# Kernel optimization log

Hardware: AMD Instinct MI355X
Metric: run time of the kernel (lower is better)

## Reference

```python
import jax, jax.numpy as jnp
import numpy as np

H, NH, KVH = 2048, 16, 4
HD = H // NH            # 128
GROUPS = NH // KVH      # 4
E, TOPK = 8, 2
I_MOE, I_SH = 1408, 5632
THETA = 1000000.0
EPS = 1e-6
B, S = 1, 1024


def rms_norm(x, w):
    var = jnp.mean(jnp.square(x), axis=-1, keepdims=True)
    return x * jax.lax.rsqrt(var + EPS) * w


def rotate_half(x):
    x1, x2 = jnp.split(x, 2, axis=-1)
    return jnp.concatenate([-x2, x1], axis=-1)


def apply_rope(q, k, position_ids):
    # q: [B,S,NH,HD], k: [B,S,KVH,HD]
    inv_freq = 1.0 / (THETA ** (jnp.arange(0, HD, 2, dtype=jnp.float32) / HD))
    ang = position_ids.astype(jnp.float32)[..., None] * inv_freq  # [B,S,HD/2]
    emb = jnp.concatenate([ang, ang], axis=-1)                    # [B,S,HD]
    cos = jnp.cos(emb)[:, :, None, :]
    sin = jnp.sin(emb)[:, :, None, :]
    q = q * cos + rotate_half(q) * sin
    k = k * cos + rotate_half(k) * sin
    return q, k


def setup_inputs() -> dict:
    key = jax.random.key(0)
    ks = jax.random.split(key, 24)
    sd = 0.02
    inp = {
        "hidden_states": jax.random.normal(ks[0], (B, S, H), jnp.float32),
        "position_ids": jnp.arange(S, dtype=jnp.int32)[None, :].repeat(B, 0),
        "ln1_w": jnp.ones((H,), jnp.float32),
        "ln2_w": jnp.ones((H,), jnp.float32),
        "q_w": jax.random.normal(ks[1], (H, NH * HD), jnp.float32) * sd,
        "q_b": jnp.zeros((NH * HD,), jnp.float32),
        "k_w": jax.random.normal(ks[2], (H, KVH * HD), jnp.float32) * sd,
        "k_b": jnp.zeros((KVH * HD,), jnp.float32),
        "v_w": jax.random.normal(ks[3], (H, KVH * HD), jnp.float32) * sd,
        "v_b": jnp.zeros((KVH * HD,), jnp.float32),
        "o_w": jax.random.normal(ks[4], (NH * HD, H), jnp.float32) * sd,
        "router_w": jax.random.normal(ks[5], (H, E), jnp.float32) * sd,
        "e_gate": jax.random.normal(ks[6], (E, H, I_MOE), jnp.float32) * sd,
        "e_up": jax.random.normal(ks[7], (E, H, I_MOE), jnp.float32) * sd,
        "e_down": jax.random.normal(ks[8], (E, I_MOE, H), jnp.float32) * sd,
        "s_gate": jax.random.normal(ks[9], (H, I_SH), jnp.float32) * sd,
        "s_up": jax.random.normal(ks[10], (H, I_SH), jnp.float32) * sd,
        "s_down": jax.random.normal(ks[11], (I_SH, H), jnp.float32) * sd,
        "sg_w": jax.random.normal(ks[12], (H, 1), jnp.float32) * sd,
    }
    return inp


def attention(x, position_ids, q_w, q_b, k_w, k_b, v_w, v_b, o_w):
    b, s, _ = x.shape
    q = (x @ q_w + q_b).reshape(b, s, NH, HD)
    k = (x @ k_w + k_b).reshape(b, s, KVH, HD)
    v = (x @ v_w + v_b).reshape(b, s, KVH, HD)
    q, k = apply_rope(q, k, position_ids)
    # GQA: repeat kv heads
    k = jnp.repeat(k, GROUPS, axis=2)  # [b,s,NH,HD]
    v = jnp.repeat(v, GROUPS, axis=2)
    scale = HD ** -0.5
    scores = jnp.einsum("bqhd,bkhd->bhqk", q, k) * scale
    causal = jnp.tril(jnp.ones((s, s), bool))
    scores = jnp.where(causal[None, None], scores, jnp.finfo(scores.dtype).min)
    probs = jax.nn.softmax(scores, axis=-1)
    out = jnp.einsum("bhqk,bkhd->bqhd", probs, v).reshape(b, s, NH * HD)
    return out @ o_w


def sparse_moe(x, router_w, e_gate, e_up, e_down, s_gate, s_up, s_down, sg_w):
    b, s, h = x.shape
    xf = x.reshape(b * s, h)  # [T,H]
    T = b * s
    probs = jax.nn.softmax(xf @ router_w, axis=-1)        # [T,E]
    top_w, top_i = jax.lax.top_k(probs, TOPK)             # norm_topk_prob=False
    weights = jnp.zeros((T, E), xf.dtype).at[jnp.arange(T)[:, None], top_i].set(top_w)
    g = jax.nn.silu(jnp.einsum("th,ehi->eti", xf, e_gate))
    u = jnp.einsum("th,ehi->eti", xf, e_up)
    d = jnp.einsum("eti,eih->eth", g * u, e_down)         # [E,T,H]
    moe_out = jnp.einsum("eth,te->th", d, weights)
    shared = (jax.nn.silu(xf @ s_gate) * (xf @ s_up)) @ s_down
    shared = shared * jax.nn.sigmoid(xf @ sg_w)
    return (moe_out + shared).reshape(b, s, h)


def reference(hidden_states, position_ids, ln1_w, ln2_w, q_w, q_b, k_w, k_b,
              v_w, v_b, o_w, router_w, e_gate, e_up, e_down,
              s_gate, s_up, s_down, sg_w):
    h = hidden_states
    attn = attention(rms_norm(h, ln1_w), position_ids,
                     q_w, q_b, k_w, k_b, v_w, v_b, o_w)
    h = h + attn
    moe = sparse_moe(rms_norm(h, ln2_w), router_w, e_gate, e_up, e_down,
                     s_gate, s_up, s_down, sg_w)
    return h + moe
```

## Files before the change

### kernel.cpp

```cpp
#include <hip/hip_runtime.h>
#include <hip/hip_bf16.h>

#define S_ 1024
#define H_ 2048
#define NH_ 16
#define KVH_ 4
#define HD_ 128
#define IM_ 1408
#define ISH_ 5632
#define E_ 8

typedef __bf16 bf16x8 __attribute__((ext_vector_type(8)));
typedef float f32x4 __attribute__((ext_vector_type(4)));

typedef unsigned int __attribute__((address_space(1))) as1_u32;
typedef unsigned int __attribute__((address_space(3))) as3_u32;

__device__ __forceinline__ void gload16(const void* g, void* l) {
  __builtin_amdgcn_global_load_lds((const as1_u32*)g, (as3_u32*)l, 16, 0, 0);
}

__device__ __forceinline__ short f2bf(float f) {
  unsigned u = __float_as_uint(f);
  u = u + 0x7FFFu + ((u >> 16) & 1u);
  return (short)(u >> 16);
}

__device__ __forceinline__ f32x4 mfma16(bf16x8 a, bf16x8 b, f32x4 c) {
  return __builtin_amdgcn_mfma_f32_16x16x32_bf16(a, b, c, 0, 0, 0);
}

template<bool MAXOP>
__device__ __forceinline__ float block_reduce(float v, float* sbuf) {
  #pragma unroll
  for (int o = 32; o >= 1; o >>= 1) {
    float t = __shfl_down(v, o);
    v = MAXOP ? fmaxf(v, t) : (v + t);
  }
  int lane = threadIdx.x & 63, w = threadIdx.x >> 6;
  if (lane == 0) sbuf[w] = v;
  __syncthreads();
  float r = sbuf[0];
  #pragma unroll
  for (int i = 1; i < 4; i++) r = MAXOP ? fmaxf(r, sbuf[i]) : (r + sbuf[i]);
  __syncthreads();
  return r;
}

struct TransDesc {
  const float* src; short* dst;
  int R, C, tx, perz, base;
  long long srcZ, dstZ;
};
struct TransAll { TransDesc d[10]; };

#define TGRP 1096

__global__ __launch_bounds__(256) void mega_k(TransAll ta, int transBlocks,
                                              const int* pos_ids, float* ct, float* st,
                                              const float* qb, const float* kb, const float* vb,
                                              float* qkv, float* attn_f, int* counts,
                                              const float* hidden, const float* ln1_w,
                                              short* x1, float* h2) {
  __shared__ float tile[4 * TGRP];
  __shared__ float sbuf[4];
  const int bid = blockIdx.x;
  const int t = threadIdx.x;
  if (bid < transBlocks) {
    int w = 0;
    #pragma unroll
    for (int i = 1; i < 10; i++) if (bid >= ta.d[i].base) w = i;
    const TransDesc& D = ta.d[w];
    int local = bid - D.base;
    int z = local / D.perz, rem = local - z * D.perz;
    int by = rem / D.tx, bx = rem - by * D.tx;
    const float* src = D.src + (long long)z * D.srcZ;
    short* dst = D.dst + (long long)z * D.dstZ;
    const int r0 = by * 64, c0 = bx * 64;
    const int C = D.C, R = D.R;
    #pragma unroll
    for (int i = 0; i < 4; i++) {
      int idx = t + i * 256;
      int row = idx >> 4, c4 = (idx & 15) * 4;
      f32x4 v = __builtin_nontemporal_load(
          (const f32x4*)&src[(size_t)(r0 + row) * C + c0 + c4]);
      *(f32x4*)&tile[(row >> 4) * TGRP + (row & 15) * 68 + c4] = v;
    }
    __syncthreads();
    const int col = t >> 2, seg = t & 3;
    const float* tp = &tile[seg * TGRP + col];
    short outv[16];
    #pragma unroll
    for (int j = 0; j < 16; j++)
      outv[j] = f2bf(tp[j * 68]);
    short* dp = &dst[(size_t)(c0 + col) * R + r0 + seg * 16];
    *(int4*)dp = *(const int4*)&outv[0];
    *(int4*)(dp + 8) = *(const int4*)&outv[8];
  } else if (bid < transBlocks + 5376) {
    int pb = bid - transBlocks;
    if (pb == 0 && t < 16) counts[t] = 0;
    if (pb < 256) {
      int i = pb * 256 + t;
      int p = i >> 6, f = i & 63;
      float pos = (float)pos_ids[p];
      float inv = powf(1.0e6f, -(float)f * (1.f / 64.f));
      float a = pos * inv;
      ct[i] = cosf(a); st[i] = sinf(a);
    } else if (pb < 3328) {
      int idx = (pb - 256) * 256 + t;
      int j = (idx * 4) % 3072;
      float4 v;
      const float* b = (j < 2048) ? qb + j : ((j < 2560) ? kb + (j - 2048) : vb + (j - 2560));
      v.x = b[0]; v.y = b[1]; v.z = b[2]; v.w = b[3];
      ((float4*)qkv)[idx] = v;
    } else {
      int idx = (pb - 3328) * 256 + t;
      ((float4*)attn_f)[idx] = (float4){0.f, 0.f, 0.f, 0.f};
    }
  } else {
    int tr = bid - transBlocks - 5376;
    const float* xr = hidden + (long long)tr * H_;
    float ss = 0.f;
    for (int i = t; i < H_ / 4; i += 256) {
      float4 v = ((const float4*)xr)[i];
      ss += v.x * v.x + v.y * v.y + v.z * v.z + v.w * v.w;
    }
    ss = block_reduce<false>(ss, sbuf);
    float rs = rsqrtf(ss * (1.f / (float)H_) + 1e-6f);
    for (int i = t; i < H_; i += 256) {
      float xv = xr[i];
      x1[(long long)tr * H_ + i] = f2bf(xv * rs * ln1_w[i]);
      h2[(long long)tr * H_ + i] = xv;
    }
  }
}

struct GemmP {
  const short* A; long long strideA; int adiv; int lda;
  const short* B; long long strideB; int bdiv; int ldb;
  void* C; long long strideC; int cdiv; int ldc;
  const int* e_off; const int* e_cnt;
  const int* list; const float* scale;
  float alpha;
  int M, N, K;
  int cskip, ckb;
  int ksplit, kchunk;
  int upoff;
};

template<int EPI>
__device__ __forceinline__ void gemm_body(const GemmP& p, int bx, int by, int bz,
                                          short* As, short* Bs) {
  constexpr bool FUSED = (EPI == 6 || EPI == 7);
  constexpr bool GATH  = (EPI == 7);
  constexpr int BM = 128, BN = 128, BK = 32;
  const int zo = bz / p.ksplit;
  const int kc = bz - zo * p.ksplit;
  const int m0 = by * BM;
  const int n0 = bx * (FUSED ? 64 : BN);
  if (FUSED && n0 >= p.N) return;

  int off = 0, cnt = p.M;
  if constexpr (EPI == 4 || GATH) {
    off = p.e_off[zo]; cnt = p.e_cnt[zo];
    if (m0 >= cnt) return;
  }
  if (p.cskip && n0 >= m0 + BM) return;
  int kend = p.ckb ? min(m0 + BM, p.K) : p.K;
  const int kbeg = kc * p.kchunk;
  kend = min(kend, kbeg + p.kchunk);
  if (kbeg >= kend) return;

  const short* Ab = p.A + (long long)(zo / p.adiv) * p.strideA;
  const short* Bb = p.B + (long long)(zo / p.bdiv) * p.strideB;

  const int tid = threadIdx.x;
  const int lane = tid & 63, wid = tid >> 6;
  const int wr = wid >> 1, wc = wid & 1;
  const int kg = lane >> 4, li = lane & 15;

  const int srow = tid >> 2;
  const int scol = (((tid & 3) ^ ((tid >> 3) & 3))) * 8;
  const short* aSrc[2];
  const short* bSrc[2];
  #pragma unroll
  for (int c = 0; c < 2; c++) {
    int ra = srow + c * 64;
    int gr;
    if constexpr (GATH)          { int rr = m0 + ra; if (rr >= cnt) rr = cnt - 1; gr = p.list[off + rr]; }
    else if constexpr (EPI == 4) { int rr = m0 + ra; if (rr >= cnt) rr = cnt - 1; gr = off + rr; }
    else                         gr = m0 + ra;
    aSrc[c] = Ab + (long long)gr * p.lda + scol;
    int br = FUSED ? (n0 + srow + (c ? p.upoff : 0)) : (n0 + srow + c * 64);
    bSrc[c] = Bb + (long long)br * p.ldb + scol;
  }

  f32x4 acc[4][4];
  #pragma unroll
  for (int i = 0; i < 4; i++)
    #pragma unroll
    for (int j = 0; j < 4; j++) acc[i][j] = (f32x4){0.f, 0.f, 0.f, 0.f};

  #pragma unroll
  for (int c = 0; c < 2; c++) {
    gload16(aSrc[c] + kbeg, &As[tid * 8 + c * 2048]);
    gload16(bSrc[c] + kbeg, &Bs[tid * 8 + c * 2048]);
  }
  __syncthreads();

  const int kgx = kg ^ ((li >> 1) & 3);
  int brow[4];
  #pragma unroll
  for (int nj = 0; nj < 4; nj++)
    brow[nj] = FUSED ? (((nj & 2) ? 64 : 0) + wc * 32 + (nj & 1) * 16 + li)
                     : (wc * 64 + nj * 16 + li);

  int cur = 0;
  for (int k0 = kbeg; k0 < kend; k0 += BK) {
    const int nk = k0 + BK;
    if (nk < kend) {
      #pragma unroll
      for (int c = 0; c < 2; c++) {
        gload16(aSrc[c] + nk, &As[(cur ^ 1) * 4096 + tid * 8 + c * 2048]);
        gload16(bSrc[c] + nk, &Bs[(cur ^ 1) * 4096 + tid * 8 + c * 2048]);
      }
    }
    bf16x8 av[4], bv[4];
    #pragma unroll
    for (int mi = 0; mi < 4; mi++)
      av[mi] = *(const bf16x8*)&As[cur * 4096 + (wr * 64 + mi * 16 + li) * BK + kgx * 8];
    #pragma unroll
    for (int nj = 0; nj < 4; nj++)
      bv[nj] = *(const bf16x8*)&Bs[cur * 4096 + brow[nj] * BK + kgx * 8];
    #pragma unroll
    for (int mi = 0; mi < 4; mi++)
      #pragma unroll
      for (int nj = 0; nj < 4; nj++)
        acc[mi][nj] = mfma16(av[mi], bv[nj], acc[mi][nj]);
    __syncthreads();
    cur ^= 1;
  }

  const long long zc = (long long)(zo / p.cdiv) * p.strideC;
  if constexpr (FUSED) {
    short* C = (short*)p.C;
    #pragma unroll
    for (int mi = 0; mi < 4; mi++) {
      #pragma unroll
      for (int nj = 0; nj < 2; nj++) {
        #pragma unroll
        for (int r = 0; r < 4; r++) {
          int ml = wr * 64 + mi * 16 + kg * 4 + r;
          int mg = m0 + ml;
          int ng = n0 + wc * 32 + nj * 16 + li;
          float g = acc[mi][nj][r], u = acc[mi][nj + 2][r];
          float gu = g * (1.f / (1.f + __expf(-g))) * u;
          if constexpr (GATH) {
            if (mg < cnt) C[(long long)(off + mg) * p.ldc + ng] = f2bf(gu);
          } else {
            C[(long long)mg * p.ldc + ng] = f2bf(gu);
          }
        }
      }
    }
  } else {
    #pragma unroll
    for (int mi = 0; mi < 4; mi++) {
      #pragma unroll
      for (int nj = 0; nj < 4; nj++) {
        #pragma unroll
        for (int r = 0; r < 4; r++) {
          int ml = wr * 64 + mi * 16 + kg * 4 + r;
          int nl2 = wc * 64 + nj * 16 + li;
          int mg = m0 + ml, ng = n0 + nl2;
          float v = acc[mi][nj][r] * p.alpha;
          if constexpr (EPI == 0) {
            float* C = (float*)p.C + zc;
            __builtin_nontemporal_store(v, &C[(long long)mg * p.ldc + ng]);
          } else if constexpr (EPI == 1) {
            float* C = (float*)p.C + zc;
            atomicAdd(&C[(long long)mg * p.ldc + ng], v);
          } else if constexpr (EPI == 4) {
            if (mg < cnt) {
              float* C = (float*)p.C;
              int tok = p.list[off + mg];
              atomicAdd(&C[(long long)tok * p.ldc + ng], p.scale[off + mg] * v);
            }
          } else if constexpr (EPI == 5) {
            float* C = (float*)p.C;
            atomicAdd(&C[(long long)mg * p.ldc + ng], p.scale[mg] * v);
          }
        }
      }
    }
  }
}

template<int EPI>
__global__ __launch_bounds__(256) void gemm_bt(GemmP p) {
  __shared__ __align__(16) short As[2 * 128 * 32];
  __shared__ __align__(16) short Bs[2 * 128 * 32];
  gemm_body<EPI>(p, blockIdx.x, blockIdx.y, blockIdx.z, As, Bs);
}

__global__ __launch_bounds__(256) void gemm_gu_dual(GemmP pe, GemmP ps) {
  __shared__ __align__(16) short As[2 * 128 * 32];
  __shared__ __align__(16) short Bs[2 * 128 * 32];
  int z = blockIdx.z;
  if (z < E_) gemm_body<7>(pe, blockIdx.x, blockIdx.y, z, As, Bs);
  else        gemm_body<6>(ps, (z - E_) * 22 + blockIdx.x, blockIdx.y, 0, As, Bs);
}

template<int EPI1, int EPI2>
__global__ __launch_bounds__(256) void gemm_dual(GemmP p1, GemmP p2, int z1) {
  __shared__ __align__(16) short As[2 * 128 * 32];
  __shared__ __align__(16) short Bs[2 * 128 * 32];
  int z = blockIdx.z;
  if (z < z1) gemm_body<EPI1>(p1, blockIdx.x, blockIdx.y, z, As, Bs);
  else        gemm_body<EPI2>(p2, blockIdx.x, blockIdx.y, z - z1, As, Bs);
}

__global__ __launch_bounds__(256) void rmsnorm_k(const float* x, const float* w, short* o,
                                                 float* copy_out, float* rs_out) {
  __shared__ float sbuf[4];
  int t = blockIdx.x;
  const float* xr = x + (long long)t * H_;
  float ss = 0.f;
  for (int i = threadIdx.x; i < H_ / 4; i += 256) {
    float4 v = ((const float4*)xr)[i];
    ss += v.x * v.x + v.y * v.y + v.z * v.z + v.w * v.w;
  }
  ss = block_reduce<false>(ss, sbuf);
  float rs = rsqrtf(ss * (1.f / (float)H_) + 1e-6f);
  for (int i = threadIdx.x; i < H_; i += 256) {
    float xv = xr[i];
    o[(long long)t * H_ + i] = f2bf(xv * rs * w[i]);
    if (copy_out) copy_out[(long long)t * H_ + i] = xv;
  }
  if (rs_out && threadIdx.x == 0) rs_out[t] = rs;
}

__global__ __launch_bounds__(256) void rope_fused_k(const float* qkv, short* qr, short* kr,
                                                    short* vt, const float* ct, const float* st) {
  int i = blockIdx.x * 256 + threadIdx.x;
  if (i < 2097152) {
    int t = i >> 11, j = i & 2047;
    int d = j & 127, f = d & 63;
    float c = ct[t * 64 + f], s = st[t * 64 + f];
    const float* row = qkv + (long long)t * 3072;
    float xv = row[j];
    float ov = (d < 64) ? -row[j + 64] : row[j - 64];
    qr[i] = f2bf(xv * c + ov * s);
  } else if (i < 2621440) {
    int j = i - 2097152;
    int t = j >> 9, jj = j & 511;
    int d = jj & 127, f = d & 63;
    float c = ct[t * 64 + f], s = st[t * 64 + f];
    const float* row = qkv + (long long)t * 3072 + 2048;
    float xv = row[jj];
    float ov = (d < 64) ? -row[jj + 64] : row[jj - 64];
    kr[j] = f2bf(xv * c + ov * s);
  } else {
    int j = i - 2621440;
    int kvh = j >> 17, rem = j & 131071;
    int d = rem >> 10, s_ = rem & 1023;
    vt[j] = f2bf(qkv[(long long)s_ * 3072 + 2560 + kvh * 128 + d]);
  }
}

__global__ __launch_bounds__(256) void cvt_bf16_k(const float* src, short* dst, int total) {
  int i = blockIdx.x * 256 + threadIdx.x;
  if (i < total) dst[i] = f2bf(src[i]);
}

__global__ __launch_bounds__(256) void softmax_k(const float* sc, short* P) {
  __shared__ float sbuf[4];
  long long row = blockIdx.x;
  int q = (int)(row & (S_ - 1));
  const float* sr = sc + row * S_;
  short* pr = P + row * S_;
  int L = q + 1;
  int Lcap = (q & ~127) + 128;
  float mx = -3.4e38f;
  for (int i = threadIdx.x; i < L; i += 256) mx = fmaxf(mx, sr[i]);
  mx = block_reduce<true>(mx, sbuf);
  float s = 0.f;
  for (int i = threadIdx.x; i < L; i += 256) s += __expf(sr[i] - mx);
  s = block_reduce<false>(s, sbuf);
  float inv = 1.f / s;
  for (int i = threadIdx.x; i < Lcap; i += 256) {
    float pv = (i < L) ? __expf(sr[i] - mx) * inv : 0.f;
    pr[i] = f2bf(pv);
  }
}

__global__ void router_k(const float* h2, const float* rs, const float* w2,
                         const float* rw, const float* sgw,
                         int* top_i, float* top_w, float* sg_sig, int* counts) {
  int t = blockIdx.x;
  int l = threadIdx.x;
  float le[8] = {0, 0, 0, 0, 0, 0, 0, 0};
  float ls = 0.f;
  float r = rs[t];
  for (int k = l; k < H_; k += 64) {
    float xv = h2[(long long)t * H_ + k] * r * w2[k];
    ls += xv * sgw[k];
    const float* rk = rw + k * E_;
    #pragma unroll
    for (int e = 0; e < E_; e++) le[e] += xv * rk[e];
  }
  #pragma unroll
  for (int o = 32; o >= 1; o >>= 1) {
    ls += __shfl_down(ls, o);
    #pragma unroll
    for (int e = 0; e < E_; e++) le[e] += __shfl_down(le[e], o);
  }
  if (l == 0) {
    float m = le[0];
    for (int e = 1; e < E_; e++) m = fmaxf(m, le[e]);
    float pe[8], s = 0.f;
    for (int e = 0; e < E_; e++) { pe[e] = __expf(le[e] - m); s += pe[e]; }
    float inv = 1.f / s;
    for (int e = 0; e < E_; e++) pe[e] *= inv;
    int i1 = 0;
    for (int e = 1; e < E_; e++) if (pe[e] > pe[i1]) i1 = e;
    int i2 = -1;
    for (int e = 0; e < E_; e++) if (e != i1 && (i2 < 0 || pe[e] > pe[i2])) i2 = e;
    top_i[2 * t] = i1; top_i[2 * t + 1] = i2;
    top_w[2 * t] = pe[i1]; top_w[2 * t + 1] = pe[i2];
    sg_sig[t] = 1.f / (1.f + __expf(-ls));
    atomicAdd(&counts[i1], 1); atomicAdd(&counts[i2], 1);
  }
}

__global__ void scan_k(const int* counts, int* offs) {
  if (threadIdx.x == 0 && blockIdx.x == 0) {
    int s = 0;
    for (int e = 0; e < E_; e++) { offs[e] = s; s += counts[e]; }
  }
}

__global__ __launch_bounds__(256) void fill_k(const int* top_i, const float* top_w, const int* offs,
                                              int* pos, int* list, float* pw) {
  int t = blockIdx.x * 256 + threadIdx.x;
  if (t >= S_) return;
  for (int j = 0; j < 2; j++) {
    int e = top_i[2 * t + j];
    int p_ = atomicAdd(&pos[e], 1);
    int slot = offs[e] + p_;
    list[slot] = t; pw[slot] = top_w[2 * t + j];
  }
}

static GemmP mkp() {
  GemmP p{};
  p.adiv = 1; p.bdiv = 1; p.cdiv = 1; p.alpha = 1.f;
  p.ksplit = 1; p.kchunk = 1 << 30;
  p.upoff = 0;
  return p;
}

extern "C" void kernel_launch(void* const* d_in, const int* in_sizes, int n_in,
                              void* d_out, int out_size, void* d_ws, size_t ws_size,
                              hipStream_t stream) {
  const float* hidden   = (const float*)d_in[0];
  const int*   pos_ids  = (const int*)d_in[1];
  const float* ln1_w    = (const float*)d_in[2];
  const float* ln2_w    = (const float*)d_in[3];
  const float* q_w      = (const float*)d_in[4];
  const float* q_b      = (const float*)d_in[5];
  const float* k_w      = (const float*)d_in[6];
  const float* k_b      = (const float*)d_in[7];
  const float* v_w      = (const float*)d_in[8];
  const float* v_b      = (const float*)d_in[9];
  const float* o_w      = (const float*)d_in[10];
  const float* router_w = (const float*)d_in[11];
  const float* e_gate   = (const float*)d_in[12];
  const float* e_up     = (const float*)d_in[13];
  const float* e_down   = (const float*)d_in[14];
  const float* s_gate   = (const float*)d_in[15];
  const float* s_up     = (const float*)d_in[16];
  const float* s_down   = (const float*)d_in[17];
  const float* sg_w     = (const float*)d_in[18];
  float* out = (float*)d_out;

  char* base = (char*)d_ws;
  size_t off_ = 0;
  auto alc = [&](size_t nbytes) -> char* {
    off_ = (off_ + 255) & ~(size_t)255;
    char* p = base + off_;
    off_ += nbytes;
    return p;
  };
  short* qkvT = (short*)alc((size_t)3072 * H_ * 2);
  short* oT   = (short*)alc((size_t)H_ * H_ * 2);
  short* eguT = (short*)alc((size_t)E_ * 2816 * H_ * 2);
  short* edT  = (short*)alc((size_t)E_ * H_ * IM_ * 2);
  short* sguT = (short*)alc((size_t)11264 * H_ * 2);
  short* sdT  = (short*)alc((size_t)H_ * ISH_ * 2);
  short* x1      = (short*)alc((size_t)S_ * H_ * 2);
  float* qkv_f   = (float*)alc((size_t)S_ * 3072 * 4);
  float* ct      = (float*)alc((size_t)S_ * 64 * 4);
  float* st      = (float*)alc((size_t)S_ * 64 * 4);
  short* qr      = (short*)alc((size_t)S_ * H_ * 2);
  short* kr      = (short*)alc((size_t)S_ * 512 * 2);
  short* vt      = (short*)alc((size_t)S_ * 512 * 2);
  float* attn_f  = (float*)alc((size_t)S_ * H_ * 4);
  short* attn    = (short*)alc((size_t)S_ * H_ * 2);
  float* h2      = (float*)alc((size_t)S_ * H_ * 4);
  short* x2      = (short*)alc((size_t)S_ * H_ * 2);
  float* rs2     = (float*)alc(S_ * 4);
  int*   top_i   = (int*)alc(2 * S_ * 4);
  float* top_w   = (float*)alc(2 * S_ * 4);
  float* sg_sig  = (float*)alc(S_ * 4);
  int*   counts  = (int*)alc(64);
  int*   pos     = counts + 8;
  int*   offs    = (int*)alc(32);
  int*   list    = (int*)alc(2 * S_ * 4);
  float* pw      = (float*)alc(2 * S_ * 4);
  char*  region  = alc(100663296);
  float* scores  = (float*)region;
  short* P       = (short*)(region + 67108864);
  short* gu_moeB = (short*)region;
  short* gushB   = (short*)(region + 16777216);

  {
    TransAll ta{};
    int b = 0;
    auto add = [&](int i, const float* s, short* d, int R, int C, int tz,
                   long long sZ, long long dZ) {
      int tx = C / 64, ty = R / 64;
      ta.d[i] = TransDesc{s, d, R, C, tx, tx * ty, b, sZ, dZ};
      b += tx * ty * tz;
    };
    add(0, q_w, qkvT, H_, H_, 1, 0, 0);
    add(1, k_w, qkvT + (size_t)2048 * H_, H_, 512, 1, 0, 0);
    add(2, v_w, qkvT + (size_t)2560 * H_, H_, 512, 1, 0, 0);
    add(3, o_w, oT, H_, H_, 1, 0, 0);
    add(4, e_gate, eguT, H_, IM_, E_, (long long)H_ * IM_, (long long)2816 * H_);
    add(5, e_up, eguT + (size_t)1408 * H_, H_, IM_, E_, (long long)H_ * IM_, (long long)2816 * H_);
    add(6, e_down, edT, IM_, H_, E_, (long long)IM_ * H_, (long long)IM_ * H_);
    add(7, s_gate, sguT, H_, ISH_, 1, 0, 0);
    add(8, s_up, sguT + (size_t)5632 * H_, H_, ISH_, 1, 0, 0);
    add(9, s_down, sdT, ISH_, H_, 1, 0, 0);
    mega_k<<<b + 5376 + 1024, 256, 0, stream>>>(ta, b, pos_ids, ct, st, q_b, k_b, v_b,
                                                qkv_f, attn_f, counts,
                                                hidden, ln1_w, x1, h2);
  }

  {
    GemmP p = mkp();
    p.A = x1; p.lda = H_;
    p.B = qkvT; p.ldb = H_;
    p.C = qkv_f; p.ldc = 3072;
    p.M = S_; p.N = 3072; p.K = H_;
    p.ksplit = 4; p.kchunk = 512;
    gemm_bt<1><<<dim3(24, 8, 4), 256, 0, stream>>>(p);
  }

  rope_fused_k<<<12288, 256, 0, stream>>>(qkv_f, qr, kr, vt, ct, st);

  {
    GemmP p = mkp();
    p.A = qr; p.strideA = HD_; p.lda = H_;
    p.B = kr; p.strideB = HD_; p.bdiv = 4; p.ldb = 512;
    p.C = scores; p.strideC = (long long)S_ * S_; p.ldc = S_;
    p.alpha = 0.08838834764831845f;
    p.M = S_; p.N = S_; p.K = HD_; p.cskip = 1;
    p.kchunk = HD_;
    gemm_bt<0><<<dim3(8, 8, NH_), 256, 0, stream>>>(p);
  }
  softmax_k<<<NH_ * S_, 256, 0, stream>>>(scores, P);
  {
    GemmP p = mkp();
    p.A = P; p.strideA = (long long)S_ * S_; p.lda = S_;
    p.B = vt; p.strideB = (long long)HD_ * S_; p.bdiv = 4; p.ldb = S_;
    p.C = attn_f; p.strideC = HD_; p.ldc = H_;
    p.M = S_; p.N = HD_; p.K = S_; p.ckb = 1;
    p.ksplit = 4; p.kchunk = 256;
    gemm_bt<1><<<dim3(1, 8, NH_ * 4), 256, 0, stream>>>(p);
  }
  cvt_bf16_k<<<8192, 256, 0, stream>>>(attn_f, attn, S_ * H_);
  {
    GemmP p = mkp();
    p.A = attn; p.lda = H_;
    p.B = oT; p.ldb = H_;
    p.C = h2; p.ldc = H_;
    p.M = S_; p.N = H_; p.K = H_;
    p.ksplit = 4; p.kchunk = 512;
    gemm_bt<1><<<dim3(16, 8, 4), 256, 0, stream>>>(p);
  }

  rmsnorm_k<<<S_, 256, 0, stream>>>(h2, ln2_w, x2, out, rs2);

  router_k<<<S_, 64, 0, stream>>>(h2, rs2, ln2_w, router_w, sg_w, top_i, top_w, sg_sig, counts);
  scan_k<<<1, 1, 0, stream>>>(counts, offs);
  fill_k<<<4, 256, 0, stream>>>(top_i, top_w, offs, pos, list, pw);

  {
    GemmP pe = mkp();
    pe.A = x2; pe.lda = H_;
    pe.B = eguT; pe.strideB = (long long)2816 * H_; pe.ldb = H_;
    pe.C = gu_moeB; pe.ldc = IM_;
    pe.e_off = offs; pe.e_cnt = counts; pe.list = list;
    pe.M = S_; pe.N = IM_; pe.K = H_;
    pe.upoff = IM_;
    GemmP ps = mkp();
    ps.A = x2; ps.lda = H_;
    ps.B = sguT; ps.ldb = H_;
    ps.C = gushB; ps.ldc = ISH_;
    ps.M = S_; ps.N = ISH_; ps.K = H_;
    ps.upoff = ISH_;
    gemm_gu_dual<<<dim3(22, 8, 12), 256, 0, stream>>>(pe, ps);
  }

  {
    GemmP pe = mkp();
    pe.A = gu_moeB; pe.lda = IM_;
    pe.B = edT; pe.strideB = (long long)H_ * IM_; pe.ldb = IM_;
    pe.C = out; pe.ldc = H_;
    pe.e_off = offs; pe.e_cnt = counts; pe.list = list; pe.scale = pw;
    pe.M = S_; pe.N = H_; pe.K = IM_;
    pe.ksplit = 2; pe.kchunk = 704;
    GemmP ps = mkp();
    ps.A = gushB; ps.lda = ISH_;
    ps.B = sdT; ps.ldb = ISH_;
    ps.C = out; ps.ldc = H_; ps.scale = sg_sig;
    ps.M = S_; ps.N = H_; ps.K = ISH_;
    ps.ksplit = 4; ps.kchunk = 1408;
    gemm_dual<4, 5><<<dim3(16, 8, E_ * 2 + 4), 256, 0, stream>>>(pe, ps, E_ * 2);
  }
}
```

Before: 615.6 us.

## Replace atomic split-K with partial buffers reduced in consumer kernels

The QKV and output-projection GEMMs now use split-K of 2 and write plain stores into two partial buffers instead of atomically accumulating into pre-initialised outputs. The bias add and residual add move into the RoPE and a new fused RMSNorm kernel, which sum the partials. The PV GEMM drops split-K and writes bf16 directly, which removes the attn_f zeroing and the separate conversion kernel. This cuts atomics, memset-style initialisation and one kernel launch, at the cost of fewer blocks per GEMM and extra partial-buffer reads.

```diff
diff --git a/kernel.cpp b/kernel.cpp
--- a/kernel.cpp
+++ b/kernel.cpp
@@ -59,9 +59,9 @@
 __global__ __launch_bounds__(256) void mega_k(TransAll ta, int transBlocks,
                                               const int* pos_ids, float* ct, float* st,
                                               const float* qb, const float* kb, const float* vb,
-                                              float* qkv, float* attn_f, int* counts,
+                                              float* biasCat, int* counts,
                                               const float* hidden, const float* ln1_w,
-                                              short* x1, float* h2) {
+                                              short* x1) {
   __shared__ float tile[4 * TGRP];
   __shared__ float sbuf[4];
   const int bid = blockIdx.x;
@@ -96,29 +96,21 @@
     short* dp = &dst[(size_t)(c0 + col) * R + r0 + seg * 16];
     *(int4*)dp = *(const int4*)&outv[0];
     *(int4*)(dp + 8) = *(const int4*)&outv[8];
-  } else if (bid < transBlocks + 5376) {
+  } else if (bid < transBlocks + 256) {
     int pb = bid - transBlocks;
-    if (pb == 0 && t < 16) counts[t] = 0;
-    if (pb < 256) {
-      int i = pb * 256 + t;
-      int p = i >> 6, f = i & 63;
-      float pos = (float)pos_ids[p];
-      float inv = powf(1.0e6f, -(float)f * (1.f / 64.f));
-      float a = pos * inv;
-      ct[i] = cosf(a); st[i] = sinf(a);
-    } else if (pb < 3328) {
-      int idx = (pb - 256) * 256 + t;
-      int j = (idx * 4) % 3072;
-      float4 v;
-      const float* b = (j < 2048) ? qb + j : ((j < 2560) ? kb + (j - 2048) : vb + (j - 2560));
-      v.x = b[0]; v.y = b[1]; v.z = b[2]; v.w = b[3];
-      ((float4*)qkv)[idx] = v;
-    } else {
-      int idx = (pb - 3328) * 256 + t;
-      ((float4*)attn_f)[idx] = (float4){0.f, 0.f, 0.f, 0.f};
+    if (pb == 0) {
+      if (t < 16) counts[t] = 0;
+      for (int j = t; j < 3072; j += 256)
+        biasCat[j] = (j < 2048) ? qb[j] : ((j < 2560) ? kb[j - 2048] : vb[j - 2560]);
     }
+    int i = pb * 256 + t;
+    int p = i >> 6, f = i & 63;
+    float pos = (float)pos_ids[p];
+    float inv = powf(1.0e6f, -(float)f * (1.f / 64.f));
+    float a = pos * inv;
+    ct[i] = cosf(a); st[i] = sinf(a);
   } else {
-    int tr = bid - transBlocks - 5376;
+    int tr = bid - transBlocks - 256;
     const float* xr = hidden + (long long)tr * H_;
     float ss = 0.f;
     for (int i = t; i < H_ / 4; i += 256) {
@@ -130,7 +122,6 @@
     for (int i = t; i < H_; i += 256) {
       float xv = xr[i];
       x1[(long long)tr * H_ + i] = f2bf(xv * rs * ln1_w[i]);
-      h2[(long long)tr * H_ + i] = xv;
     }
   }
 }
@@ -275,11 +266,11 @@
           int mg = m0 + ml, ng = n0 + nl2;
           float v = acc[mi][nj][r] * p.alpha;
           if constexpr (EPI == 0) {
-            float* C = (float*)p.C + zc;
-            __builtin_nontemporal_store(v, &C[(long long)mg * p.ldc + ng]);
-          } else if constexpr (EPI == 1) {
-            float* C = (float*)p.C + zc;
-            atomicAdd(&C[(long long)mg * p.ldc + ng], v);
+            float* C = (float*)p.C + zc + (long long)kc * p.strideC;
+            C[(long long)mg * p.ldc + ng] = v;
+          } else if constexpr (EPI == 2) {
+            short* C = (short*)p.C + zc;
+            C[(long long)mg * p.ldc + ng] = f2bf(v);
           } else if constexpr (EPI == 4) {
             if (mg < cnt) {
               float* C = (float*)p.C;
@@ -320,57 +311,61 @@
   else        gemm_body<EPI2>(p2, blockIdx.x, blockIdx.y, z - z1, As, Bs);
 }
 
-__global__ __launch_bounds__(256) void rmsnorm_k(const float* x, const float* w, short* o,
-                                                 float* copy_out, float* rs_out) {
-  __shared__ float sbuf[4];
-  int t = blockIdx.x;
-  const float* xr = x + (long long)t * H_;
-  float ss = 0.f;
-  for (int i = threadIdx.x; i < H_ / 4; i += 256) {
-    float4 v = ((const float4*)xr)[i];
-    ss += v.x * v.x + v.y * v.y + v.z * v.z + v.w * v.w;
-  }
-  ss = block_reduce<false>(ss, sbuf);
-  float rs = rsqrtf(ss * (1.f / (float)H_) + 1e-6f);
-  for (int i = threadIdx.x; i < H_; i += 256) {
-    float xv = xr[i];
-    o[(long long)t * H_ + i] = f2bf(xv * rs * w[i]);
-    if (copy_out) copy_out[(long long)t * H_ + i] = xv;
-  }
-  if (rs_out && threadIdx.x == 0) rs_out[t] = rs;
-}
-
-__global__ __launch_bounds__(256) void rope_fused_k(const float* qkv, short* qr, short* kr,
+__global__ __launch_bounds__(256) void rope_fused_k(const float* p0, const float* p1,
+                                                    const float* bias, short* qr, short* kr,
                                                     short* vt, const float* ct, const float* st) {
   int i = blockIdx.x * 256 + threadIdx.x;
   if (i < 2097152) {
     int t = i >> 11, j = i & 2047;
     int d = j & 127, f = d & 63;
     float c = ct[t * 64 + f], s = st[t * 64 + f];
-    const float* row = qkv + (long long)t * 3072;
-    float xv = row[j];
-    float ov = (d < 64) ? -row[j + 64] : row[j - 64];
+    long long base = (long long)t * 3072;
+    float xv = p0[base + j] + p1[base + j] + bias[j];
+    int jo = (d < 64) ? j + 64 : j - 64;
+    float ov = p0[base + jo] + p1[base + jo] + bias[jo];
+    if (d < 64) ov = -ov;
     qr[i] = f2bf(xv * c + ov * s);
   } else if (i < 2621440) {
     int j = i - 2097152;
     int t = j >> 9, jj = j & 511;
     int d = jj & 127, f = d & 63;
     float c = ct[t * 64 + f], s = st[t * 64 + f];
-    const float* row = qkv + (long long)t * 3072 + 2048;
-    float xv = row[jj];
-    float ov = (d < 64) ? -row[jj + 64] : row[jj - 64];
+    long long base = (long long)t * 3072 + 2048;
+    float xv = p0[base + jj] + p1[base + jj] + bias[2048 + jj];
+    int jo = (d < 64) ? jj + 64 : jj - 64;
+    float ov = p0[base + jo] + p1[base + jo] + bias[2048 + jo];
+    if (d < 64) ov = -ov;
     kr[j] = f2bf(xv * c + ov * s);
   } else {
     int j = i - 2621440;
     int kvh = j >> 17, rem = j & 131071;
     int d = rem >> 10, s_ = rem & 1023;
-    vt[j] = f2bf(qkv[(long long)s_ * 3072 + 2560 + kvh * 128 + d]);
-  }
-}
-
-__global__ __launch_bounds__(256) void cvt_bf16_k(const float* src, short* dst, int total) {
-  int i = blockIdx.x * 256 + threadIdx.x;
-  if (i < total) dst[i] = f2bf(src[i]);
+    long long idx = (long long)s_ * 3072 + 2560 + kvh * 128 + d;
+    vt[j] = f2bf(p0[idx] + p1[idx] + bias[2560 + kvh * 128 + d]);
+  }
+}
+
+__global__ __launch_bounds__(256) void rmsnorm2f_k(const float* p0, const float* p1,
+                                                   const float* hid, const float* w,
+                                                   short* x2, float* outp, float* rs_out) {
+  __shared__ float rowbuf[H_];
+  __shared__ float sbuf[4];
+  int tr = blockIdx.x;
+  long long base = (long long)tr * H_;
+  float ss = 0.f;
+  for (int i = threadIdx.x; i < H_; i += 256) {
+    float hv = p0[base + i] + p1[base + i] + hid[base + i];
+    rowbuf[i] = hv;
+    ss += hv * hv;
+  }
+  ss = block_reduce<false>(ss, sbuf);
+  float rs = rsqrtf(ss * (1.f / (float)H_) + 1e-6f);
+  for (int i = threadIdx.x; i < H_; i += 256) {
+    float hv = rowbuf[i];
+    outp[base + i] = hv;
+    x2[base + i] = f2bf(hv * rs * w[i]);
+  }
+  if (threadIdx.x == 0) rs_out[tr] = rs;
 }
 
 __global__ __launch_bounds__(256) void softmax_k(const float* sc, short* P) {
@@ -499,15 +494,15 @@
   short* sguT = (short*)alc((size_t)11264 * H_ * 2);
   short* sdT  = (short*)alc((size_t)H_ * ISH_ * 2);
   short* x1      = (short*)alc((size_t)S_ * H_ * 2);
-  float* qkv_f   = (float*)alc((size_t)S_ * 3072 * 4);
+  float* qkv_p   = (float*)alc((size_t)2 * S_ * 3072 * 4);
+  float* o_part  = (float*)alc((size_t)2 * S_ * H_ * 4);
+  float* biasCat = (float*)alc(3072 * 4);
   float* ct      = (float*)alc((size_t)S_ * 64 * 4);
   float* st      = (float*)alc((size_t)S_ * 64 * 4);
   short* qr      = (short*)alc((size_t)S_ * H_ * 2);
   short* kr      = (short*)alc((size_t)S_ * 512 * 2);
   short* vt      = (short*)alc((size_t)S_ * 512 * 2);
-  float* attn_f  = (float*)alc((size_t)S_ * H_ * 4);
   short* attn    = (short*)alc((size_t)S_ * H_ * 2);
-  float* h2      = (float*)alc((size_t)S_ * H_ * 4);
   short* x2      = (short*)alc((size_t)S_ * H_ * 2);
   float* rs2     = (float*)alc(S_ * 4);
   int*   top_i   = (int*)alc(2 * S_ * 4);
@@ -543,22 +538,22 @@
     add(7, s_gate, sguT, H_, ISH_, 1, 0, 0);
     add(8, s_up, sguT + (size_t)5632 * H_, H_, ISH_, 1, 0, 0);
     add(9, s_down, sdT, ISH_, H_, 1, 0, 0);
-    mega_k<<<b + 5376 + 1024, 256, 0, stream>>>(ta, b, pos_ids, ct, st, q_b, k_b, v_b,
-                                                qkv_f, attn_f, counts,
-                                                hidden, ln1_w, x1, h2);
+    mega_k<<<b + 256 + 1024, 256, 0, stream>>>(ta, b, pos_ids, ct, st, q_b, k_b, v_b,
+                                               biasCat, counts, hidden, ln1_w, x1);
   }
 
   {
     GemmP p = mkp();
     p.A = x1; p.lda = H_;
     p.B = qkvT; p.ldb = H_;
-    p.C = qkv_f; p.ldc = 3072;
+    p.C = qkv_p; p.strideC = (long long)S_ * 3072; p.ldc = 3072;
     p.M = S_; p.N = 3072; p.K = H_;
-    p.ksplit = 4; p.kchunk = 512;
-    gemm_bt<1><<<dim3(24, 8, 4), 256, 0, stream>>>(p);
-  }
-
-  rope_fused_k<<<12288, 256, 0, stream>>>(qkv_f, qr, kr, vt, ct, st);
+    p.ksplit = 2; p.kchunk = 1024;
+    gemm_bt<0><<<dim3(24, 8, 2), 256, 0, stream>>>(p);
+  }
+
+  rope_fused_k<<<12288, 256, 0, stream>>>(qkv_p, qkv_p + (size_t)S_ * 3072, biasCat,
+                                          qr, kr, vt, ct, st);
 
   {
     GemmP p = mkp();
@@ -567,7 +562,6 @@
     p.C = scores; p.strideC = (long long)S_ * S_; p.ldc = S_;
     p.alpha = 0.08838834764831845f;
     p.M = S_; p.N = S_; p.K = HD_; p.cskip = 1;
-    p.kchunk = HD_;
     gemm_bt<0><<<dim3(8, 8, NH_), 256, 0, stream>>>(p);
   }
   softmax_k<<<NH_ * S_, 256, 0, stream>>>(scores, P);
@@ -575,25 +569,24 @@
     GemmP p = mkp();
     p.A = P; p.strideA = (long long)S_ * S_; p.lda = S_;
     p.B = vt; p.strideB = (long long)HD_ * S_; p.bdiv = 4; p.ldb = S_;
-    p.C = attn_f; p.strideC = HD_; p.ldc = H_;
+    p.C = attn; p.strideC = HD_; p.ldc = H_;
     p.M = S_; p.N = HD_; p.K = S_; p.ckb = 1;
-    p.ksplit = 4; p.kchunk = 256;
-    gemm_bt<1><<<dim3(1, 8, NH_ * 4), 256, 0, stream>>>(p);
-  }
-  cvt_bf16_k<<<8192, 256, 0, stream>>>(attn_f, attn, S_ * H_);
+    gemm_bt<2><<<dim3(1, 8, NH_), 256, 0, stream>>>(p);
+  }
   {
     GemmP p = mkp();
     p.A = attn; p.lda = H_;
     p.B = oT; p.ldb = H_;
-    p.C = h2; p.ldc = H_;
+    p.C = o_part; p.strideC = (long long)S_ * H_; p.ldc = H_;
     p.M = S_; p.N = H_; p.K = H_;
-    p.ksplit = 4; p.kchunk = 512;
-    gemm_bt<1><<<dim3(16, 8, 4), 256, 0, stream>>>(p);
-  }
-
-  rmsnorm_k<<<S_, 256, 0, stream>>>(h2, ln2_w, x2, out, rs2);
-
-  router_k<<<S_, 64, 0, stream>>>(h2, rs2, ln2_w, router_w, sg_w, top_i, top_w, sg_sig, counts);
+    p.ksplit = 2; p.kchunk = 1024;
+    gemm_bt<0><<<dim3(16, 8, 2), 256, 0, stream>>>(p);
+  }
+
+  rmsnorm2f_k<<<S_, 256, 0, stream>>>(o_part, o_part + (size_t)S_ * H_, hidden,
+                                      ln2_w, x2, out, rs2);
+
+  router_k<<<S_, 64, 0, stream>>>(out, rs2, ln2_w, router_w, sg_w, top_i, top_w, sg_sig, counts);
   scan_k<<<1, 1, 0, stream>>>(counts, offs);
   fill_k<<<4, 256, 0, stream>>>(top_i, top_w, offs, pos, list, pw);
 
```

Measured after the change: 553.6 us. -10.1%, faster.
